# Kernel optimization log

Hardware: AMD Instinct MI355X
Metric: run time of the kernel (lower is better)

Reference implementation:

```python
import math
import jax, jax.numpy as jnp
import numpy as np

B, I, G, C, D = 8192, 512, 32, 16, 32  # batch, dim_input, groups, num_components, dim_output
CD = C * D


def setup_inputs() -> dict:
    key = jax.random.key(0)
    ks = jax.random.split(key, 8)
    bound = 1.0 / math.sqrt(I)

    def unif(k, shape):
        return jax.random.uniform(k, shape, jnp.float32, -bound, bound)

    x = jax.random.normal(ks[0], (B, I), jnp.float32)
    # soft group-mixture weights (rows sum to 1, as produced upstream)
    g = jax.nn.softmax(jax.random.normal(ks[1], (B, G), jnp.float32), axis=-1)
    return {
        "x": x,
        "g": g,
        "W_mu": unif(ks[2], (G, I, CD)),
        "b_mu": unif(ks[3], (G, CD)),
        "W_sigma": unif(ks[4], (G, I, CD)),
        "b_sigma": unif(ks[5], (G, CD)),
        "W_pi": unif(ks[6], (G, I, C)),
        "b_pi": unif(ks[7], (G, C)),
    }


def _group_linear(x, g, W, b):
    # Fused form of: w_b = (g @ W.reshape(G, I*O)).reshape(B, I, O); x[:,None,:] @ w_b + g @ b
    # einsum avoids materializing the [B, I, O] per-sample weight tensor.
    return jnp.einsum("bi,gio,bg->bo", x, W, g) + g @ b


def reference(x, g, W_mu, b_mu, W_sigma, b_sigma, W_pi, b_pi):
    logits = _group_linear(x, g, W_pi, b_pi)                      # [B, C]
    loc = _group_linear(x, g, W_mu, b_mu)                         # [B, C*D]
    scale = jax.nn.softplus(_group_linear(x, g, W_sigma, b_sigma)) + 1e-7  # [B, C*D]
    # GroupGMM returns a MixtureSameFamily parameterized by (logits, loc, scale);
    # we return the concatenated parameter tensor [B, C + 2*C*D].
    return jnp.concatenate([logits, loc, scale], axis=-1)
```

## Files before the change

### kernel.cpp

```cpp
#include <hip/hip_runtime.h>
#include <hip/hip_bf16.h>

#define BATCH 8192
#define IDIM  512
#define GDIM  32
#define NOUT  1040
#define NPAD  1152
#define KW    16384
#define BM    128
#define BN    128
#define KQ    128

typedef short bf16x8 __attribute__((ext_vector_type(8)));
typedef float floatx4 __attribute__((ext_vector_type(4)));

typedef const __attribute__((address_space(1))) unsigned short gus_t;
typedef __attribute__((address_space(3))) unsigned short lus_t;

__device__ inline unsigned pk2(float a, float b) {
    union { __hip_bfloat162 h2; unsigned u; } cv;
    cv.h2 = __float22bfloat162_rn(float2{a, b});
    return cv.u;
}

__global__ void cvt_bf16(const float* __restrict__ s, unsigned short* __restrict__ d) {
    int t = blockIdx.x * 256 + threadIdx.x;
    const float4* sp = (const float4*)s + (size_t)t * 2;
    float4 a = sp[0], b = sp[1];
    uint4 p;
    p.x = pk2(a.x, a.y); p.y = pk2(a.z, a.w);
    p.z = pk2(b.x, b.y); p.w = pk2(b.z, b.w);
    *(uint4*)(d + (size_t)t * 8) = p;
}

__global__ void prep_wt(const float* __restrict__ Wmu, const float* __restrict__ Wsig,
                        const float* __restrict__ Wpi, unsigned short* __restrict__ Wt) {
    int n = blockIdx.y * 256 + threadIdx.x;
    if (n >= NPAD) return;
    int k0 = blockIdx.x * 8;
    float v[8];
#pragma unroll
    for (int j = 0; j < 8; ++j) {
        int k = k0 + j, gg = k >> 9, i = k & 511;
        float val = 0.0f;
        if (n < 16)         val = Wpi [(gg * 512 + i) * 16  + n];
        else if (n < 528)   val = Wmu [(gg * 512 + i) * 512 + (n - 16)];
        else if (n < NOUT)  val = Wsig[(gg * 512 + i) * 512 + (n - 528)];
        v[j] = val;
    }
    uint4 p;
    p.x = pk2(v[0], v[1]); p.y = pk2(v[2], v[3]);
    p.z = pk2(v[4], v[5]); p.w = pk2(v[6], v[7]);
    const int col = n >> 7, r = n & 127;
    const int h = r >> 6, tn = (r >> 4) & 3, l15 = r & 15;
    const int kk = k0 >> 5, q = (k0 >> 3) & 3;
    size_t idx = ((size_t)(col * 512 + kk) << 12) + ((((h * 4 + tn) * 4 + q) * 16 + l15) * 8);
    *(uint4*)&Wt[idx] = p;
}

__global__ void prep_wb(const float* __restrict__ bmu, const float* __restrict__ bsig,
                        const float* __restrict__ bpi, unsigned short* __restrict__ Wb) {
    int n = blockIdx.y * 256 + threadIdx.x;
    if (n >= NPAD) return;
    int k0 = blockIdx.x * 8;
    float v[8];
#pragma unroll
    for (int j = 0; j < 8; ++j) {
        int gg = k0 + j;
        float val = 0.0f;
        if (n < 16)         val = bpi [gg * 16  + n];
        else if (n < 528)   val = bmu [gg * 512 + (n - 16)];
        else if (n < NOUT)  val = bsig[gg * 512 + (n - 528)];
        v[j] = val;
    }
    uint4 p;
    p.x = pk2(v[0], v[1]); p.y = pk2(v[2], v[3]);
    p.z = pk2(v[4], v[5]); p.w = pk2(v[6], v[7]);
    *(uint4*)&Wb[(size_t)n * GDIM + k0] = p;
}

__global__ __launch_bounds__(256, 2) void gemm_gmm(
        const unsigned short* __restrict__ xb, const unsigned short* __restrict__ gb,
        const float* __restrict__ g, const unsigned short* __restrict__ Wt,
        const unsigned short* __restrict__ Wb, float* __restrict__ out) {
    __shared__ unsigned short lA[BM * KQ];
    __shared__ unsigned short bufB[2 * 4096];
    __shared__ float ratL[GDIM * BM];
    __shared__ float g31L[BM];

    const int t = threadIdx.x, lane = t & 63, w = t >> 6;
    const int wm = (w & 1) * 64, wn = (w >> 1) * 64;
    const int h = w >> 1;
    const int q = lane >> 4, l15 = lane & 15;

    const int bx = blockIdx.x;
    const int seq = (bx & 7) * 72 + (bx >> 3);
    const int col = seq >> 6, mblk = seq & 63;
    const int m0 = mblk * BM, n0 = col * BN;

    const unsigned short* WtCol = Wt + ((size_t)col * 512 << 12);

    floatx4 acc[4][4] = {};
    bf16x8 af[4][4];
    floatx4 r4[4];
    const int swA = l15 & 7;

    auto stageB = [&](int s, int p) {
        const int kg = (((s >> 2) & 31) << 4) + ((s >> 7) << 2) + (s & 3);
        const unsigned short* src = WtCol + ((size_t)kg << 12) + t * 8;
        unsigned short* dst = &bufB[p * 4096 + t * 8];
        __builtin_amdgcn_global_load_lds((gus_t*)src,        (lus_t*)dst,        16, 0, 0);
        __builtin_amdgcn_global_load_lds((gus_t*)(src+2048), (lus_t*)(dst+2048), 16, 0, 0);
    };
    auto loadR = [&](int gg) {
#pragma unroll
        for (int tm = 0; tm < 4; ++tm)
            r4[tm] = *(const floatx4*)&ratL[gg * BM + wm + tm * 16 + q * 4];
    };

    stageB(0, 0); stageB(1, 1);

#pragma unroll
    for (int j = 0; j < 16; ++j) {
        int idx = t + 256 * j;
        int gg = idx >> 7, row = idx & 127;
        float cur  = g[(size_t)(m0 + row) * GDIM + gg];
        float prev = g[(size_t)(m0 + row) * GDIM + ((gg + 31) & 31)];
        ratL[idx] = prev / cur;
    }
    if (t < BM) g31L[t] = g[(size_t)(m0 + t) * GDIM + 31];
    __syncthreads();
    loadR(0);

    for (int kb = 0; kb < 4; ++kb) {
        __syncthreads();
        {
            const int r = t >> 1;
            const unsigned short* src = xb + (size_t)(m0 + r) * IDIM + kb * KQ + (t & 1) * 64;
#pragma unroll
            for (int j = 0; j < 8; ++j) {
                int gi = (t & 1) * 8 + j;
                uint4 v = *(const uint4*)(src + j * 8);
                *(uint4*)&lA[(r * 16 + (gi ^ (r & 7))) * 8] = v;
            }
        }
        __syncthreads();

#pragma unroll
        for (int ks = 0; ks < 4; ++ks)
#pragma unroll
            for (int tm = 0; tm < 4; ++tm)
                af[ks][tm] = *(const bf16x8*)
                    &lA[((wm + tm * 16 + l15) * 16 + ((ks * 4 + q) ^ swA)) * 8];

        for (int gg = 0; gg < GDIM; ++gg) {
            const int flat = kb * GDIM + gg;
            const int sbase = flat * 4;
            const bool lastgg = (kb == 3) && (gg == 31);

#pragma unroll
            for (int tm = 0; tm < 4; ++tm)
#pragma unroll
                for (int tn = 0; tn < 4; ++tn)
#pragma unroll
                    for (int r = 0; r < 4; ++r)
                        acc[tm][tn][r] *= r4[tm][r];

#pragma unroll
            for (int ks = 0; ks < 4; ++ks) {
                const int p = ks & 1;
                if (ks == 3) { if (lastgg) asm volatile("s_waitcnt vmcnt(0)" ::: "memory");
                               else        asm volatile("s_waitcnt vmcnt(2)" ::: "memory"); }
                else                       asm volatile("s_waitcnt vmcnt(2)" ::: "memory");
                __builtin_amdgcn_sched_barrier(0);
                __builtin_amdgcn_s_barrier();

                bf16x8 bfr[4];
#pragma unroll
                for (int tn = 0; tn < 4; ++tn)
                    bfr[tn] = *(const bf16x8*)
                        &bufB[p * 4096 + (((h * 4 + tn) * 4 + q) * 16 + l15) * 8];
                asm volatile("s_waitcnt lgkmcnt(0)" ::: "memory");
                __builtin_amdgcn_sched_barrier(0);
                __builtin_amdgcn_s_barrier();

                const int s2 = sbase + ks + 2;
                if (s2 < 512) stageB(s2, p);

#pragma unroll
                for (int tm = 0; tm < 4; ++tm)
#pragma unroll
                    for (int tn = 0; tn < 4; ++tn)
                        acc[tm][tn] = __builtin_amdgcn_mfma_f32_16x16x32_bf16(
                            af[ks][tm], bfr[tn], acc[tm][tn], 0, 0, 0);
            }
            loadR((gg + 1) & 31);
        }
    }

#pragma unroll
    for (int tm = 0; tm < 4; ++tm) {
        floatx4 gl = *(const floatx4*)&g31L[wm + tm * 16 + q * 4];
#pragma unroll
        for (int tn = 0; tn < 4; ++tn)
#pragma unroll
            for (int r = 0; r < 4; ++r)
                acc[tm][tn][r] *= gl[r];
    }

    __syncthreads();
    {
        const int r = t >> 1;
        const unsigned short* src = gb + (size_t)(m0 + r) * GDIM + (t & 1) * 16;
        *(uint4*)&lA[r * 40 + (t & 1) * 16]     = *(const uint4*)(src);
        *(uint4*)&lA[r * 40 + (t & 1) * 16 + 8] = *(const uint4*)(src + 8);
    }
    __syncthreads();
    {
        bf16x8 afb[4], bb[4];
#pragma unroll
        for (int tm = 0; tm < 4; ++tm)
            afb[tm] = *(const bf16x8*)&lA[(wm + tm * 16 + l15) * 40 + q * 8];
#pragma unroll
        for (int tn = 0; tn < 4; ++tn)
            bb[tn] = *(const bf16x8*)(Wb + (size_t)(n0 + wn + tn * 16 + l15) * GDIM + q * 8);
#pragma unroll
        for (int tm = 0; tm < 4; ++tm)
#pragma unroll
            for (int tn = 0; tn < 4; ++tn)
                acc[tm][tn] = __builtin_amdgcn_mfma_f32_16x16x32_bf16(
                    afb[tm], bb[tn], acc[tm][tn], 0, 0, 0);
    }

#pragma unroll
    for (int tn = 0; tn < 4; ++tn) {
        int n = n0 + wn + tn * 16 + l15;
        if (n >= NOUT) continue;
        bool is_scale = (n >= 528);
#pragma unroll
        for (int tm = 0; tm < 4; ++tm) {
            int mbase = m0 + wm + tm * 16 + q * 4;
#pragma unroll
            for (int r = 0; r < 4; ++r) {
                float vv = acc[tm][tn][r];
                if (is_scale) {
                    float sp = (vv > 15.0f) ? vv : log1pf(expf(vv));
                    vv = sp + 1e-7f;
                }
                out[(size_t)(mbase + r) * NOUT + n] = vv;
            }
        }
    }
}

extern "C" void kernel_launch(void* const* d_in, const int* in_sizes, int n_in,
                              void* d_out, int out_size, void* d_ws, size_t ws_size,
                              hipStream_t stream) {
    const float* x    = (const float*)d_in[0];
    const float* g    = (const float*)d_in[1];
    const float* Wmu  = (const float*)d_in[2];
    const float* bmu  = (const float*)d_in[3];
    const float* Wsig = (const float*)d_in[4];
    const float* bsig = (const float*)d_in[5];
    const float* Wpi  = (const float*)d_in[6];
    const float* bpi  = (const float*)d_in[7];
    float* out = (float*)d_out;

    char* ws = (char*)d_ws;
    unsigned short* Wt = (unsigned short*)ws;  ws += (size_t)NPAD * KW * 2;
    unsigned short* xb = (unsigned short*)ws;  ws += (size_t)BATCH * IDIM * 2;
    unsigned short* gb = (unsigned short*)ws;  ws += (size_t)BATCH * GDIM * 2;
    unsigned short* Wb = (unsigned short*)ws;

    cvt_bf16<<<BATCH * IDIM / 2048, 256, 0, stream>>>(x, xb);
    cvt_bf16<<<BATCH * GDIM / 2048, 256, 0, stream>>>(g, gb);
    prep_wt<<<dim3(KW / 8, 5), 256, 0, stream>>>(Wmu, Wsig, Wpi, Wt);
    prep_wb<<<dim3(GDIM / 8, 5), 256, 0, stream>>>(bmu, bsig, bpi, Wb);
    gemm_gmm<<<(BATCH / BM) * (NPAD / BN), 256, 0, stream>>>(xb, gb, g, Wt, Wb, out);
}
```

Baseline: 588.6 us.

## Give each wave a private B-tile pipeline to drop block-wide barriers

Each wave now stages its own half of the weight tile into per-wave LDS slabs, replacing the shared double buffer. This removes the two s_barrier calls per k-step, and the next B fragments are read into registers one step ahead. The prep kernel applies an XOR swizzle on the lane index to avoid LDS bank conflicts, and the g[:,31] scaling now reads global memory directly instead of a shared array. The cost is duplicated B loads: both waves sharing a column half fetch the same data, so global and L2 traffic doubles and LDS use grows. Correctness also depends on the per-wave vmcnt accounting.

```diff
diff --git a/kernel.cpp b/kernel.cpp
--- a/kernel.cpp
+++ b/kernel.cpp
@@ -54,7 +54,8 @@
     const int col = n >> 7, r = n & 127;
     const int h = r >> 6, tn = (r >> 4) & 3, l15 = r & 15;
     const int kk = k0 >> 5, q = (k0 >> 3) & 3;
-    size_t idx = ((size_t)(col * 512 + kk) << 12) + ((((h * 4 + tn) * 4 + q) * 16 + l15) * 8);
+    const int l15s = l15 ^ (q << 1);
+    size_t idx = ((size_t)(col * 512 + kk) << 12) + ((((h * 4 + tn) * 4 + q) * 16 + l15s) * 8);
     *(uint4*)&Wt[idx] = p;
 }
 
@@ -84,9 +85,8 @@
         const float* __restrict__ g, const unsigned short* __restrict__ Wt,
         const unsigned short* __restrict__ Wb, float* __restrict__ out) {
     __shared__ unsigned short lA[BM * KQ];
-    __shared__ unsigned short bufB[2 * 4096];
+    __shared__ unsigned short bufB[4 * 2 * 2048];
     __shared__ float ratL[GDIM * BM];
-    __shared__ float g31L[BM];
 
     const int t = threadIdx.x, lane = t & 63, w = t >> 6;
     const int wm = (w & 1) * 64, wn = (w >> 1) * 64;
@@ -102,15 +102,24 @@
 
     floatx4 acc[4][4] = {};
     bf16x8 af[4][4];
+    bf16x8 bfr[2][4];
     floatx4 r4[4];
     const int swA = l15 & 7;
 
-    auto stageB = [&](int s, int p) {
+    auto stageB = [&](int s, int slab) {
         const int kg = (((s >> 2) & 31) << 4) + ((s >> 7) << 2) + (s & 3);
-        const unsigned short* src = WtCol + ((size_t)kg << 12) + t * 8;
-        unsigned short* dst = &bufB[p * 4096 + t * 8];
-        __builtin_amdgcn_global_load_lds((gus_t*)src,        (lus_t*)dst,        16, 0, 0);
-        __builtin_amdgcn_global_load_lds((gus_t*)(src+2048), (lus_t*)(dst+2048), 16, 0, 0);
+        const unsigned short* src = WtCol + ((size_t)kg << 12) + h * 2048 + lane * 8;
+        unsigned short* dst = &bufB[(w * 2 + slab) * 2048 + lane * 8];
+#pragma unroll
+        for (int i = 0; i < 4; ++i)
+            __builtin_amdgcn_global_load_lds((gus_t*)(src + i * 512),
+                                             (lus_t*)(dst + i * 512), 16, 0, 0);
+    };
+    auto readB = [&](int slab, bf16x8* d) {
+#pragma unroll
+        for (int tn = 0; tn < 4; ++tn)
+            d[tn] = *(const bf16x8*)
+                &bufB[(w * 2 + slab) * 2048 + ((tn * 4 + q) * 16 + (l15 ^ (q << 1))) * 8];
     };
     auto loadR = [&](int gg) {
 #pragma unroll
@@ -128,9 +137,9 @@
         float prev = g[(size_t)(m0 + row) * GDIM + ((gg + 31) & 31)];
         ratL[idx] = prev / cur;
     }
-    if (t < BM) g31L[t] = g[(size_t)(m0 + t) * GDIM + 31];
     __syncthreads();
     loadR(0);
+    readB(0, bfr[0]);
 
     for (int kb = 0; kb < 4; ++kb) {
         __syncthreads();
@@ -154,10 +163,6 @@
                     &lA[((wm + tm * 16 + l15) * 16 + ((ks * 4 + q) ^ swA)) * 8];
 
         for (int gg = 0; gg < GDIM; ++gg) {
-            const int flat = kb * GDIM + gg;
-            const int sbase = flat * 4;
-            const bool lastgg = (kb == 3) && (gg == 31);
-
 #pragma unroll
             for (int tm = 0; tm < 4; ++tm)
 #pragma unroll
@@ -168,45 +173,34 @@
 
 #pragma unroll
             for (int ks = 0; ks < 4; ++ks) {
-                const int p = ks & 1;
-                if (ks == 3) { if (lastgg) asm volatile("s_waitcnt vmcnt(0)" ::: "memory");
-                               else        asm volatile("s_waitcnt vmcnt(2)" ::: "memory"); }
-                else                       asm volatile("s_waitcnt vmcnt(2)" ::: "memory");
-                __builtin_amdgcn_sched_barrier(0);
-                __builtin_amdgcn_s_barrier();
-
-                bf16x8 bfr[4];
-#pragma unroll
-                for (int tn = 0; tn < 4; ++tn)
-                    bfr[tn] = *(const bf16x8*)
-                        &bufB[p * 4096 + (((h * 4 + tn) * 4 + q) * 16 + l15) * 8];
+                const int s = (kb * GDIM + gg) * 4 + ks;
+                const int cur = ks & 1;
                 asm volatile("s_waitcnt lgkmcnt(0)" ::: "memory");
                 __builtin_amdgcn_sched_barrier(0);
-                __builtin_amdgcn_s_barrier();
-
-                const int s2 = sbase + ks + 2;
-                if (s2 < 512) stageB(s2, p);
-
+                stageB((s + 2) & 511, cur);
+                asm volatile("s_waitcnt vmcnt(4)" ::: "memory");
+                __builtin_amdgcn_sched_barrier(0);
+                readB(cur ^ 1, bfr[cur ^ 1]);
 #pragma unroll
                 for (int tm = 0; tm < 4; ++tm)
 #pragma unroll
                     for (int tn = 0; tn < 4; ++tn)
                         acc[tm][tn] = __builtin_amdgcn_mfma_f32_16x16x32_bf16(
-                            af[ks][tm], bfr[tn], acc[tm][tn], 0, 0, 0);
+                            af[ks][tm], bfr[cur][tn], acc[tm][tn], 0, 0, 0);
             }
             loadR((gg + 1) & 31);
         }
     }
 
 #pragma unroll
-    for (int tm = 0; tm < 4; ++tm) {
-        floatx4 gl = *(const floatx4*)&g31L[wm + tm * 16 + q * 4];
-#pragma unroll
-        for (int tn = 0; tn < 4; ++tn)
-#pragma unroll
-            for (int r = 0; r < 4; ++r)
-                acc[tm][tn][r] *= gl[r];
-    }
+    for (int tm = 0; tm < 4; ++tm)
+#pragma unroll
+        for (int r = 0; r < 4; ++r) {
+            float gv = g[(size_t)(m0 + wm + tm * 16 + q * 4 + r) * GDIM + 31];
+#pragma unroll
+            for (int tn = 0; tn < 4; ++tn)
+                acc[tm][tn][r] *= gv;
+        }
 
     __syncthreads();
     {
```

After: 562.8 us. 4.4% less time.
